# Performance work log

Hardware: AMD Instinct MI355X
Metric: run time of the kernel (lower is better)

## Reference

```python
import jax, jax.numpy as jnp
import numpy as np

B, H, S, D = 1, 16, 2048, 128
WINDOW = 512  # sliding-window size (SWA)
NEG = -1e9


def _swa_mask(s):
    # causal sliding-window additive mask: 0 where attended, -1e9 otherwise
    i = jnp.arange(s)[:, None]
    j = jnp.arange(s)[None, :]
    allowed = (j <= i) & (j > i - WINDOW)
    return jnp.where(allowed, 0.0, NEG).astype(jnp.float32)[None, None]  # [1,1,S,S]


def setup_inputs() -> dict:
    key = jax.random.key(0)
    kq, kk, kv = jax.random.split(key, 3)
    q = jax.random.normal(kq, (B, H, S, D), dtype=jnp.float32)
    k = jax.random.normal(kk, (B, H, S, D), dtype=jnp.float32)
    v = jax.random.normal(kv, (B, H, S, D), dtype=jnp.float32)
    mask = _swa_mask(S)
    return {"q": q, "k": k, "v": v, "mask": mask}


def reference(q, k, v, mask):
    # attn_w = q @ k^T + mask; softmax over kv; @ v  (no scaling, per source)
    attn_w = jnp.einsum("bhqd,bhkd->bhqk", q, k) + mask
    attn_w = jax.nn.softmax(attn_w, axis=-1)
    return jnp.einsum("bhqk,bhkd->bhqd", attn_w, v)
```

## Files before the change

kernel.cpp:

```cpp
#include <hip/hip_runtime.h>
#include <hip/hip_bf16.h>
#include <stdint.h>

#define H_NUM 16
#define S_LEN 2048
#define D_DIM 128
#define WIN   512
#define NWG   256
#define LOG2E 1.4426950408889634f

typedef __attribute__((ext_vector_type(8)))  _Float16 half8;
typedef __attribute__((ext_vector_type(2)))  __fp16   fp16x2;
typedef __attribute__((ext_vector_type(16))) float f32x16;
typedef __attribute__((ext_vector_type(4)))  unsigned int uint4v;

static __device__ __forceinline__ uint32_t pk16(float a, float b) {
    fp16x2 t = __builtin_amdgcn_cvt_pkrtz(a, b);
    return __builtin_bit_cast(uint32_t, t);
}
static __device__ __forceinline__ float fexp2(float x) {
#if __has_builtin(__builtin_amdgcn_exp2f)
    return __builtin_amdgcn_exp2f(x);
#else
    return exp2f(x);
#endif
}

__global__ __launch_bounds__(512, 2) void swa_fwd(
    const float* __restrict__ Q, const float* __restrict__ K,
    const float* __restrict__ V, float* __restrict__ O)
{
    __shared__ __align__(16) char arena[71680];
    char* ksL = arena;
    char* vsL = arena + 16384;
    char* ksH = arena + 32768;
    char* vsH = arena + 49152;
    float* mrg_o  = (float*)arena;
    float* mrg_ml = (float*)(arena + 69632);

    int bid = blockIdx.x;
    int wid = ((bid & 7) << 5) | (bid >> 3);
    int h    = wid >> 4;
    int q0wg = (wid & 15) << 7;

    int tid  = threadIdx.x;
    int wv   = tid >> 6;
    int lane = tid & 63;
    int qn = lane & 31;
    int hi = lane >> 5;
    int qsel = wv & 3;
    int hseg = wv >> 2;
    int q0 = q0wg + qsel * 32;

    const float* Qh = Q + ((size_t)h << 18);
    const float* Kg = K + ((size_t)h << 18);
    const float* Vg = V + ((size_t)h << 18);
    float*       Oh = O + ((size_t)h << 18);

    int tK_r = tid >> 4;
    int tK_d = (tid & 15) * 8;
    int tK_byte = tK_r * 256 + (((tid & 15) * 16) ^ ((tK_r & 7) << 4));
    int tV_d = (tid >> 4) * 4;
    int tV_s = (tid & 15) * 2;
    int tV_byte = (tV_s >> 3) * 2048 + tV_d * 16 + (tV_s & 7) * 2;

#define K_LOAD(A0, A1, KB_) do {                                               \
        const float* sp_ = Kg + ((size_t)((KB_) + tK_r) << 7) + tK_d;          \
        A0 = *reinterpret_cast<const float4*>(sp_);                            \
        A1 = *reinterpret_cast<const float4*>(sp_ + 4); } while (0)
#define K_WRITE(KS, BUF, A0, A1) do {                                          \
        uint4v u_;                                                             \
        u_[0] = pk16(A0.x, A0.y); u_[1] = pk16(A0.z, A0.w);                    \
        u_[2] = pk16(A1.x, A1.y); u_[3] = pk16(A1.z, A1.w);                    \
        *reinterpret_cast<uint4v*>((KS) + (BUF) * 8192 + tK_byte) = u_; } while (0)
#define V_LOAD(A0, A1, KB_) do {                                               \
        const float* sp_ = Vg + ((size_t)((KB_) + tV_s) << 7) + tV_d;          \
        A0 = *reinterpret_cast<const float4*>(sp_);                            \
        A1 = *reinterpret_cast<const float4*>(sp_ + D_DIM); } while (0)
#define V_WRITE(VS, BUF, A0, A1) do {                                          \
        char* b_ = (VS) + (BUF) * 8192 + tV_byte;                              \
        *reinterpret_cast<uint32_t*>(b_)      = pk16(A0.x, A1.x);              \
        *reinterpret_cast<uint32_t*>(b_ + 16) = pk16(A0.y, A1.y);              \
        *reinterpret_cast<uint32_t*>(b_ + 32) = pk16(A0.z, A1.z);              \
        *reinterpret_cast<uint32_t*>(b_ + 48) = pk16(A0.w, A1.w); } while (0)

    half8 qa[8];
    const float* qrow = Qh + ((size_t)(q0 + qn) << 7) + hi * 8;
    #pragma unroll
    for (int c = 0; c < 8; ++c) {
        float4 a0 = *reinterpret_cast<const float4*>(qrow + c * 16);
        float4 a1 = *reinterpret_cast<const float4*>(qrow + c * 16 + 4);
        qa[c] = (half8){(_Float16)(a0.x * LOG2E), (_Float16)(a0.y * LOG2E),
                        (_Float16)(a0.z * LOG2E), (_Float16)(a0.w * LOG2E),
                        (_Float16)(a1.x * LOG2E), (_Float16)(a1.y * LOG2E),
                        (_Float16)(a1.z * LOG2E), (_Float16)(a1.w * LOG2E)};
    }

    f32x16 oacc[4];
    #pragma unroll
    for (int db = 0; db < 4; ++db)
        #pragma unroll
        for (int i = 0; i < 16; ++i) oacc[db][i] = 0.f;
    float m_s = -1e30f, l_s = 0.f;

    int kstart = q0wg - (WIN - 1);
    if (kstart < 0) kstart = 0;
    kstart &= ~31;
    int nt  = ((q0wg + 128) - kstart) >> 5;
    int nt0 = (nt + 1) >> 1;
    int ntH = nt - nt0;
    int iq   = q0 + qn;
    int w_ks = q0 - (WIN - 1);
    int w_ke = q0 + 32;

    {
        float4 a0, a1;
        K_LOAD(a0, a1, kstart);             K_WRITE(ksL, 0, a0, a1);
        K_LOAD(a0, a1, kstart + nt0 * 32);  K_WRITE(ksH, 0, a0, a1);
        V_LOAD(a0, a1, kstart);             V_WRITE(vsL, 0, a0, a1);
        V_LOAD(a0, a1, kstart + nt0 * 32);  V_WRITE(vsH, 0, a0, a1);
    }

    int my_cnt = hseg ? ntH : nt0;
    for (int it = 0; it < nt0; ++it) {
        int cur = it & 1, nxt = cur ^ 1;
        __syncthreads();

        bool hl = (it + 1 < nt0), hh = (it + 1 < ntH);
        float4 kl0, kl1, kh0, kh1;
        if (hl) K_LOAD(kl0, kl1, kstart + (it + 1) * 32);
        if (hh) K_LOAD(kh0, kh1, kstart + (nt0 + it + 1) * 32);

        int mt = (hseg ? nt0 : 0) + it;
        int kb = kstart + mt * 32;
        bool act = (it < my_cnt) && (kb < w_ke) && (kb + 32 > w_ks);
        const char* ksb = (hseg ? ksH : ksL) + cur * 8192;
        const char* vsb = (hseg ? vsH : vsL) + cur * 8192;

        f32x16 sacc;
        if (act) {
            #pragma unroll
            for (int i = 0; i < 16; ++i) sacc[i] = 0.f;
            int sw = (qn & 7) << 4;
            #pragma unroll
            for (int c = 0; c < 8; ++c) {
                half8 kh = *reinterpret_cast<const half8*>(
                    ksb + qn * 256 + ((c * 32 + hi * 16) ^ sw));
                sacc = __builtin_amdgcn_mfma_f32_32x32x16_f16(kh, qa[c], sacc, 0, 0, 0);
            }
        }

        if (hl) K_WRITE(ksL, nxt, kl0, kl1);
        if (hh) K_WRITE(ksH, nxt, kh0, kh1);
        float4 vl0, vl1, vh0, vh1;
        if (hl) V_LOAD(vl0, vl1, kstart + (it + 1) * 32);
        if (hh) V_LOAD(vh0, vh1, kstart + (nt0 + it + 1) * 32);

        if (act) {
            float p[16];
            bool fullt = (kb >= q0 - 480) && (kb <= q0 - 31);
            if (fullt) {
                #pragma unroll
                for (int r = 0; r < 16; ++r) p[r] = sacc[r];
            } else {
                #pragma unroll
                for (int r = 0; r < 16; ++r) {
                    int j = kb + (r & 3) + 8 * (r >> 2) + 4 * hi;
                    p[r] = ((j <= iq) && (j + WIN > iq)) ? sacc[r] : -1e30f;
                }
            }
            float t0 = fmaxf(fmaxf(p[0], p[1]), p[2]);
            float t1 = fmaxf(fmaxf(p[3], p[4]), p[5]);
            float t2 = fmaxf(fmaxf(p[6], p[7]), p[8]);
            float t3 = fmaxf(fmaxf(p[9], p[10]), p[11]);
            float t4 = fmaxf(fmaxf(p[12], p[13]), p[14]);
            float tm = fmaxf(fmaxf(fmaxf(t0, t1), fmaxf(t2, t3)), fmaxf(t4, p[15]));
            tm = fmaxf(tm, __shfl_xor(tm, 32));

            if (!__all(tm - m_s <= 11.5424f)) {
                float mn = fmaxf(m_s, tm);
                float scale = fexp2(m_s - mn);
                m_s = mn;
                l_s *= scale;
                #pragma unroll
                for (int r = 0; r < 16; ++r) {
                    float sr = __shfl(scale, (r & 3) + 8 * (r >> 2) + 4 * hi);
                    oacc[0][r] *= sr; oacc[1][r] *= sr;
                    oacc[2][r] *= sr; oacc[3][r] *= sr;
                }
            }
            #pragma unroll
            for (int r = 0; r < 16; ++r) p[r] = fexp2(p[r] - m_s);
            {
                float s0 = (p[0] + p[1]) + (p[2] + p[3]);
                float s1 = (p[4] + p[5]) + (p[6] + p[7]);
                float s2 = (p[8] + p[9]) + (p[10] + p[11]);
                float s3 = (p[12] + p[13]) + (p[14] + p[15]);
                l_s += (s0 + s1) + (s2 + s3);
            }

            half8 pa[2];
            #pragma unroll
            for (int c = 0; c < 2; ++c) {
                uint32_t u0 = pk16(p[8*c+0], p[8*c+1]);
                uint32_t u1 = pk16(p[8*c+2], p[8*c+3]);
                uint32_t u2 = pk16(p[8*c+4], p[8*c+5]);
                uint32_t u3 = pk16(p[8*c+6], p[8*c+7]);
                uint4v fw;
#if __has_builtin(__builtin_amdgcn_permlane32_swap)
                auto w02 = __builtin_amdgcn_permlane32_swap(u0, u2, false, false);
                auto w13 = __builtin_amdgcn_permlane32_swap(u1, u3, false, false);
                fw[0] = (uint32_t)w02[0]; fw[2] = (uint32_t)w02[1];
                fw[1] = (uint32_t)w13[0]; fw[3] = (uint32_t)w13[1];
#else
                uint32_t x0 = (uint32_t)__shfl_xor((int)u0, 32);
                uint32_t x1 = (uint32_t)__shfl_xor((int)u1, 32);
                uint32_t x2 = (uint32_t)__shfl_xor((int)u2, 32);
                uint32_t x3 = (uint32_t)__shfl_xor((int)u3, 32);
                if (hi == 0) { fw[0] = u0; fw[1] = u1; fw[2] = x0; fw[3] = x1; }
                else         { fw[0] = x2; fw[1] = x3; fw[2] = u2; fw[3] = u3; }
#endif
                pa[c] = __builtin_bit_cast(half8, fw);
            }

            #pragma unroll
            for (int db = 0; db < 4; ++db)
                #pragma unroll
                for (int c = 0; c < 2; ++c) {
                    half8 vb8 = *reinterpret_cast<const half8*>(
                        vsb + (2 * c + hi) * 2048 + (db * 32 + qn) * 16);
                    oacc[db] = __builtin_amdgcn_mfma_f32_32x32x16_f16(pa[c], vb8, oacc[db], 0, 0, 0);
                }
        }

        if (hl) V_WRITE(vsL, nxt, vl0, vl1);
        if (hh) V_WRITE(vsH, nxt, vh0, vh1);
    }

    l_s += __shfl_xor(l_s, 32);
    __syncthreads();

    if (hseg == 1) {
        float* mo = mrg_o + (size_t)(qsel * 64 + lane) * 68;
        #pragma unroll
        for (int db = 0; db < 4; ++db)
            #pragma unroll
            for (int r = 0; r < 16; ++r) mo[db * 16 + r] = oacc[db][r];
        mrg_ml[(qsel * 64 + lane) * 2 + 0] = m_s;
        mrg_ml[(qsel * 64 + lane) * 2 + 1] = l_s;
    }
    __syncthreads();
    if (hseg == 0) {
        float m1 = mrg_ml[(qsel * 64 + lane) * 2 + 0];
        float l1 = mrg_ml[(qsel * 64 + lane) * 2 + 1];
        float mm = fmaxf(m_s, m1);
        float e0 = fexp2(m_s - mm);
        float e1 = fexp2(m1 - mm);
        float inv = 1.f / (l_s * e0 + l1 * e1);
        float sc0 = e0 * inv, sc1 = e1 * inv;
        const float* mo = mrg_o + (size_t)(qsel * 64 + lane) * 68;
        #pragma unroll
        for (int r = 0; r < 16; ++r) {
            int qr = (r & 3) + 8 * (r >> 2) + 4 * hi;
            float s0r = __shfl(sc0, qr);
            float s1r = __shfl(sc1, qr);
            float* orow = Oh + ((size_t)(q0 + qr) << 7) + qn;
            #pragma unroll
            for (int db = 0; db < 4; ++db)
                orow[db * 32] = oacc[db][r] * s0r + mo[db * 16 + r] * s1r;
        }
    }
#undef K_LOAD
#undef K_WRITE
#undef V_LOAD
#undef V_WRITE
}

extern "C" void kernel_launch(void* const* d_in, const int* in_sizes, int n_in,
                              void* d_out, int out_size, void* d_ws, size_t ws_size,
                              hipStream_t stream) {
    (void)in_sizes; (void)n_in; (void)out_size; (void)d_ws; (void)ws_size;
    const float* q = (const float*)d_in[0];
    const float* k = (const float*)d_in[1];
    const float* v = (const float*)d_in[2];
    float* o = (float*)d_out;
    hipLaunchKernelGGL(swa_fwd, dim3(NWG), dim3(512), 0, stream, q, k, v, o);
}
```

Before: 32.58 us.

## Process 64-key KV tiles per iteration instead of 32 in SWA kernel

Each loop iteration now loads, stages and consumes two 32-row K/V sub-tiles, for a 64-key tile. It issues two QK MFMA chains and four PV MFMA steps per d-block. This halves the number of barriers and loop iterations and gives more independent MFMA work between syncs. In exchange, LDS use grows to 128 KB, the kernel holds twice as many prefetch and probability registers under the same 512-thread launch bound (risking spills), and 64-alignment of the window start can add partially masked work.

Measured after the change: 54.87 us. +68.4%, slower.

```diff
diff --git a/kernel.cpp b/kernel.cpp
--- a/kernel.cpp
+++ b/kernel.cpp
@@ -30,11 +30,11 @@
     const float* __restrict__ Q, const float* __restrict__ K,
     const float* __restrict__ V, float* __restrict__ O)
 {
-    __shared__ __align__(16) char arena[71680];
+    __shared__ __align__(16) char arena[131072];
     char* ksL = arena;
-    char* vsL = arena + 16384;
-    char* ksH = arena + 32768;
-    char* vsH = arena + 49152;
+    char* vsL = arena + 32768;
+    char* ksH = arena + 65536;
+    char* vsH = arena + 98304;
     float* mrg_o  = (float*)arena;
     float* mrg_ml = (float*)(arena + 69632);
 
@@ -64,21 +64,21 @@
     int tV_s = (tid & 15) * 2;
     int tV_byte = (tV_s >> 3) * 2048 + tV_d * 16 + (tV_s & 7) * 2;
 
-#define K_LOAD(A0, A1, KB_) do {                                               \
-        const float* sp_ = Kg + ((size_t)((KB_) + tK_r) << 7) + tK_d;          \
+#define K_LOAD(A0, A1, KB_, SUB) do {                                          \
+        const float* sp_ = Kg + ((size_t)((KB_) + 32*(SUB) + tK_r) << 7) + tK_d;\
         A0 = *reinterpret_cast<const float4*>(sp_);                            \
         A1 = *reinterpret_cast<const float4*>(sp_ + 4); } while (0)
-#define K_WRITE(KS, BUF, A0, A1) do {                                          \
+#define K_WRITE(KS, BUF, A0, A1, SUB) do {                                     \
         uint4v u_;                                                             \
         u_[0] = pk16(A0.x, A0.y); u_[1] = pk16(A0.z, A0.w);                    \
         u_[2] = pk16(A1.x, A1.y); u_[3] = pk16(A1.z, A1.w);                    \
-        *reinterpret_cast<uint4v*>((KS) + (BUF) * 8192 + tK_byte) = u_; } while (0)
-#define V_LOAD(A0, A1, KB_) do {                                               \
-        const float* sp_ = Vg + ((size_t)((KB_) + tV_s) << 7) + tV_d;          \
+        *reinterpret_cast<uint4v*>((KS) + (BUF) * 16384 + (SUB) * 8192 + tK_byte) = u_; } while (0)
+#define V_LOAD(A0, A1, KB_, SUB) do {                                          \
+        const float* sp_ = Vg + ((size_t)((KB_) + 32*(SUB) + tV_s) << 7) + tV_d;\
         A0 = *reinterpret_cast<const float4*>(sp_);                            \
         A1 = *reinterpret_cast<const float4*>(sp_ + D_DIM); } while (0)
-#define V_WRITE(VS, BUF, A0, A1) do {                                          \
-        char* b_ = (VS) + (BUF) * 8192 + tV_byte;                              \
+#define V_WRITE(VS, BUF, A0, A1, SUB) do {                                     \
+        char* b_ = (VS) + (BUF) * 16384 + (SUB) * 8192 + tV_byte;              \
         *reinterpret_cast<uint32_t*>(b_)      = pk16(A0.x, A1.x);              \
         *reinterpret_cast<uint32_t*>(b_ + 16) = pk16(A0.y, A1.y);              \
         *reinterpret_cast<uint32_t*>(b_ + 32) = pk16(A0.z, A1.z);              \
@@ -105,8 +105,8 @@
 
     int kstart = q0wg - (WIN - 1);
     if (kstart < 0) kstart = 0;
-    kstart &= ~31;
-    int nt  = ((q0wg + 128) - kstart) >> 5;
+    kstart &= ~63;
+    int nt  = ((q0wg + 128) - kstart) >> 6;
     int nt0 = (nt + 1) >> 1;
     int ntH = nt - nt0;
     int iq   = q0 + qn;
@@ -115,10 +115,14 @@
 
     {
         float4 a0, a1;
-        K_LOAD(a0, a1, kstart);             K_WRITE(ksL, 0, a0, a1);
-        K_LOAD(a0, a1, kstart + nt0 * 32);  K_WRITE(ksH, 0, a0, a1);
-        V_LOAD(a0, a1, kstart);             V_WRITE(vsL, 0, a0, a1);
-        V_LOAD(a0, a1, kstart + nt0 * 32);  V_WRITE(vsH, 0, a0, a1);
+        K_LOAD(a0, a1, kstart, 0);             K_WRITE(ksL, 0, a0, a1, 0);
+        K_LOAD(a0, a1, kstart, 1);             K_WRITE(ksL, 0, a0, a1, 1);
+        K_LOAD(a0, a1, kstart + nt0 * 64, 0);  K_WRITE(ksH, 0, a0, a1, 0);
+        K_LOAD(a0, a1, kstart + nt0 * 64, 1);  K_WRITE(ksH, 0, a0, a1, 1);
+        V_LOAD(a0, a1, kstart, 0);             V_WRITE(vsL, 0, a0, a1, 0);
+        V_LOAD(a0, a1, kstart, 1);             V_WRITE(vsL, 0, a0, a1, 1);
+        V_LOAD(a0, a1, kstart + nt0 * 64, 0);  V_WRITE(vsH, 0, a0, a1, 0);
+        V_LOAD(a0, a1, kstart + nt0 * 64, 1);  V_WRITE(vsH, 0, a0, a1, 1);
     }
 
     int my_cnt = hseg ? ntH : nt0;
@@ -127,46 +131,64 @@
         __syncthreads();
 
         bool hl = (it + 1 < nt0), hh = (it + 1 < ntH);
-        float4 kl0, kl1, kh0, kh1;
-        if (hl) K_LOAD(kl0, kl1, kstart + (it + 1) * 32);
-        if (hh) K_LOAD(kh0, kh1, kstart + (nt0 + it + 1) * 32);
+        float4 kl0a, kl1a, kl0b, kl1b, kh0a, kh1a, kh0b, kh1b;
+        if (hl) { K_LOAD(kl0a, kl1a, kstart + (it + 1) * 64, 0);
+                  K_LOAD(kl0b, kl1b, kstart + (it + 1) * 64, 1); }
+        if (hh) { K_LOAD(kh0a, kh1a, kstart + (nt0 + it + 1) * 64, 0);
+                  K_LOAD(kh0b, kh1b, kstart + (nt0 + it + 1) * 64, 1); }
 
         int mt = (hseg ? nt0 : 0) + it;
-        int kb = kstart + mt * 32;
-        bool act = (it < my_cnt) && (kb < w_ke) && (kb + 32 > w_ks);
-        const char* ksb = (hseg ? ksH : ksL) + cur * 8192;
-        const char* vsb = (hseg ? vsH : vsL) + cur * 8192;
-
-        f32x16 sacc;
+        int kb = kstart + mt * 64;
+        bool act = (it < my_cnt) && (kb < w_ke) && (kb + 64 > w_ks);
+        const char* ksb = (hseg ? ksH : ksL) + cur * 16384;
+        const char* vsb = (hseg ? vsH : vsL) + cur * 16384;
+
+        f32x16 sacc0, sacc1;
         if (act) {
             #pragma unroll
-            for (int i = 0; i < 16; ++i) sacc[i] = 0.f;
+            for (int i = 0; i < 16; ++i) { sacc0[i] = 0.f; sacc1[i] = 0.f; }
             int sw = (qn & 7) << 4;
             #pragma unroll
             for (int c = 0; c < 8; ++c) {
-                half8 kh = *reinterpret_cast<const half8*>(
+                half8 ka = *reinterpret_cast<const half8*>(
                     ksb + qn * 256 + ((c * 32 + hi * 16) ^ sw));
-                sacc = __builtin_amdgcn_mfma_f32_32x32x16_f16(kh, qa[c], sacc, 0, 0, 0);
+                half8 kbq = *reinterpret_cast<const half8*>(
+                    ksb + 8192 + qn * 256 + ((c * 32 + hi * 16) ^ sw));
+                sacc0 = __builtin_amdgcn_mfma_f32_32x32x16_f16(ka,  qa[c], sacc0, 0, 0, 0);
+                sacc1 = __builtin_amdgcn_mfma_f32_32x32x16_f16(kbq, qa[c], sacc1, 0, 0, 0);
             }
         }
 
-        if (hl) K_WRITE(ksL, nxt, kl0, kl1);
-        if (hh) K_WRITE(ksH, nxt, kh0, kh1);
-        float4 vl0, vl1, vh0, vh1;
-        if (hl) V_LOAD(vl0, vl1, kstart + (it + 1) * 32);
-        if (hh) V_LOAD(vh0, vh1, kstart + (nt0 + it + 1) * 32);
+        if (hl) { K_WRITE(ksL, nxt, kl0a, kl1a, 0); K_WRITE(ksL, nxt, kl0b, kl1b, 1); }
+        if (hh) { K_WRITE(ksH, nxt, kh0a, kh1a, 0); K_WRITE(ksH, nxt, kh0b, kh1b, 1); }
+        float4 vl0a, vl1a, vl0b, vl1b, vh0a, vh1a, vh0b, vh1b;
+        if (hl) { V_LOAD(vl0a, vl1a, kstart + (it + 1) * 64, 0);
+                  V_LOAD(vl0b, vl1b, kstart + (it + 1) * 64, 1); }
+        if (hh) { V_LOAD(vh0a, vh1a, kstart + (nt0 + it + 1) * 64, 0);
+                  V_LOAD(vh0b, vh1b, kstart + (nt0 + it + 1) * 64, 1); }
 
         if (act) {
-            float p[16];
-            bool fullt = (kb >= q0 - 480) && (kb <= q0 - 31);
-            if (fullt) {
-                #pragma unroll
-                for (int r = 0; r < 16; ++r) p[r] = sacc[r];
+            float p[32];
+            bool full0 = (kb      >= q0 - 480) && (kb      <= q0 - 31);
+            bool full1 = (kb + 32 >= q0 - 480) && (kb + 32 <= q0 - 31);
+            if (full0) {
+                #pragma unroll
+                for (int r = 0; r < 16; ++r) p[r] = sacc0[r];
             } else {
                 #pragma unroll
                 for (int r = 0; r < 16; ++r) {
                     int j = kb + (r & 3) + 8 * (r >> 2) + 4 * hi;
-                    p[r] = ((j <= iq) && (j + WIN > iq)) ? sacc[r] : -1e30f;
+                    p[r] = ((j <= iq) && (j + WIN > iq)) ? sacc0[r] : -1e30f;
+                }
+            }
+            if (full1) {
+                #pragma unroll
+                for (int r = 0; r < 16; ++r) p[16 + r] = sacc1[r];
+            } else {
+                #pragma unroll
+                for (int r = 0; r < 16; ++r) {
+                    int j = kb + 32 + (r & 3) + 8 * (r >> 2) + 4 * hi;
+                    p[16 + r] = ((j <= iq) && (j + WIN > iq)) ? sacc1[r] : -1e30f;
                 }
             }
             float t0 = fmaxf(fmaxf(p[0], p[1]), p[2]);
@@ -174,7 +196,15 @@
             float t2 = fmaxf(fmaxf(p[6], p[7]), p[8]);
             float t3 = fmaxf(fmaxf(p[9], p[10]), p[11]);
             float t4 = fmaxf(fmaxf(p[12], p[13]), p[14]);
-            float tm = fmaxf(fmaxf(fmaxf(t0, t1), fmaxf(t2, t3)), fmaxf(t4, p[15]));
+            float t5 = fmaxf(fmaxf(p[15], p[16]), p[17]);
+            float t6 = fmaxf(fmaxf(p[18], p[19]), p[20]);
+            float t7 = fmaxf(fmaxf(p[21], p[22]), p[23]);
+            float t8 = fmaxf(fmaxf(p[24], p[25]), p[26]);
+            float t9 = fmaxf(fmaxf(p[27], p[28]), p[29]);
+            float ta = fmaxf(p[30], p[31]);
+            float tm = fmaxf(fmaxf(fmaxf(fmaxf(t0, t1), fmaxf(t2, t3)),
+                                   fmaxf(fmaxf(t4, t5), fmaxf(t6, t7))),
+                             fmaxf(fmaxf(t8, t9), ta));
             tm = fmaxf(tm, __shfl_xor(tm, 32));
 
             if (!__all(tm - m_s <= 11.5424f)) {
@@ -190,51 +220,60 @@
                 }
             }
             #pragma unroll
-            for (int r = 0; r < 16; ++r) p[r] = fexp2(p[r] - m_s);
+            for (int r = 0; r < 32; ++r) p[r] = fexp2(p[r] - m_s);
             {
                 float s0 = (p[0] + p[1]) + (p[2] + p[3]);
                 float s1 = (p[4] + p[5]) + (p[6] + p[7]);
                 float s2 = (p[8] + p[9]) + (p[10] + p[11]);
                 float s3 = (p[12] + p[13]) + (p[14] + p[15]);
-                l_s += (s0 + s1) + (s2 + s3);
-            }
-
-            half8 pa[2];
-            #pragma unroll
-            for (int c = 0; c < 2; ++c) {
-                uint32_t u0 = pk16(p[8*c+0], p[8*c+1]);
-                uint32_t u1 = pk16(p[8*c+2], p[8*c+3]);
-                uint32_t u2 = pk16(p[8*c+4], p[8*c+5]);
-                uint32_t u3 = pk16(p[8*c+6], p[8*c+7]);
-                uint4v fw;
+                float s4 = (p[16] + p[17]) + (p[18] + p[19]);
+                float s5 = (p[20] + p[21]) + (p[22] + p[23]);
+                float s6 = (p[24] + p[25]) + (p[26] + p[27]);
+                float s7 = (p[28] + p[29]) + (p[30] + p[31]);
+                l_s += ((s0 + s1) + (s2 + s3)) + ((s4 + s5) + (s6 + s7));
+            }
+
+            half8 pa[4];
+            #pragma unroll
+            for (int s = 0; s < 2; ++s)
+                #pragma unroll
+                for (int c = 0; c < 2; ++c) {
+                    const float* ps = p + 16 * s + 8 * c;
+                    uint32_t u0 = pk16(ps[0], ps[1]);
+                    uint32_t u1 = pk16(ps[2], ps[3]);
+                    uint32_t u2 = pk16(ps[4], ps[5]);
+                    uint32_t u3 = pk16(ps[6], ps[7]);
+                    uint4v fw;
 #if __has_builtin(__builtin_amdgcn_permlane32_swap)
-                auto w02 = __builtin_amdgcn_permlane32_swap(u0, u2, false, false);
-                auto w13 = __builtin_amdgcn_permlane32_swap(u1, u3, false, false);
-                fw[0] = (uint32_t)w02[0]; fw[2] = (uint32_t)w02[1];
-                fw[1] = (uint32_t)w13[0]; fw[3] = (uint32_t)w13[1];
+                    auto w02 = __builtin_amdgcn_permlane32_swap(u0, u2, false, false);
+                    auto w13 = __builtin_amdgcn_permlane32_swap(u1, u3, false, false);
+                    fw[0] = (uint32_t)w02[0]; fw[2] = (uint32_t)w02[1];
+                    fw[1] = (uint32_t)w13[0]; fw[3] = (uint32_t)w13[1];
 #else
-                uint32_t x0 = (uint32_t)__shfl_xor((int)u0, 32);
-                uint32_t x1 = (uint32_t)__shfl_xor((int)u1, 32);
-                uint32_t x2 = (uint32_t)__shfl_xor((int)u2, 32);
-                uint32_t x3 = (uint32_t)__shfl_xor((int)u3, 32);
-                if (hi == 0) { fw[0] = u0; fw[1] = u1; fw[2] = x0; fw[3] = x1; }
-                else         { fw[0] = x2; fw[1] = x3; fw[2] = u2; fw[3] = u3; }
+                    uint32_t x0 = (uint32_t)__shfl_xor((int)u0, 32);
+                    uint32_t x1 = (uint32_t)__shfl_xor((int)u1, 32);
+                    uint32_t x2 = (uint32_t)__shfl_xor((int)u2, 32);
+                    uint32_t x3 = (uint32_t)__shfl_xor((int)u3, 32);
+                    if (hi == 0) { fw[0] = u0; fw[1] = u1; fw[2] = x0; fw[3] = x1; }
+                    else         { fw[0] = x2; fw[1] = x3; fw[2] = u2; fw[3] = u3; }
 #endif
-                pa[c] = __builtin_bit_cast(half8, fw);
-            }
+                    pa[2 * s + c] = __builtin_bit_cast(half8, fw);
+                }
 
             #pragma unroll
             for (int db = 0; db < 4; ++db)
                 #pragma unroll
-                for (int c = 0; c < 2; ++c) {
-                    half8 vb8 = *reinterpret_cast<const half8*>(
-                        vsb + (2 * c + hi) * 2048 + (db * 32 + qn) * 16);
-                    oacc[db] = __builtin_amdgcn_mfma_f32_32x32x16_f16(pa[c], vb8, oacc[db], 0, 0, 0);
-                }
+                for (int s = 0; s < 2; ++s)
+                    #pragma unroll
+                    for (int c = 0; c < 2; ++c) {
+                        half8 vb8 = *reinterpret_cast<const half8*>(
+                            vsb + s * 8192 + (2 * c + hi) * 2048 + (db * 32 + qn) * 16);
+                        oacc[db] = __builtin_amdgcn_mfma_f32_32x32x16_f16(pa[2*s+c], vb8, oacc[db], 0, 0, 0);
+                    }
         }
 
-        if (hl) V_WRITE(vsL, nxt, vl0, vl1);
-        if (hh) V_WRITE(vsH, nxt, vh0, vh1);
+        if (hl) { V_WRITE(vsL, nxt, vl0a, vl1a, 0); V_WRITE(vsL, nxt, vl0b, vl1b, 1); }
+        if (hh) { V_WRITE(vsH, nxt, vh0a, vh1a, 0); V_WRITE(vsH, nxt, vh0b, vh1b, 1); }
     }
 
     l_s += __shfl_xor(l_s, 32);
```

## Software-pipeline QK^T of next tile with softmax/PV of previous tile

Applied to the files above, without the earlier changes.

Restructures the KV loop so that the QK^T MFMAs and the V register loads for tile i are issued alongside the softmax and PV MFMAs of tile i-1, with a final drain after the loop. The aim is to overlap matrix-core work with the exp/max vector work and to hide LDS latency by prefetching V into registers. In exchange it raises register pressure by keeping an extra score accumulator and 8 V fragments live, which may lower occupancy. It also removes the full-tile mask fast path and the lazy-rescale skip, so masking and rescaling now run on every tile.

Result: slower. 67.39 us (+106.8%).

```diff
diff --git a/kernel.cpp b/kernel.cpp
--- a/kernel.cpp
+++ b/kernel.cpp
@@ -113,6 +113,99 @@
     int w_ks = q0 - (WIN - 1);
     int w_ke = q0 + 32;
 
+    f32x16 saccP;
+    #pragma unroll
+    for (int i = 0; i < 16; ++i) saccP[i] = 0.f;
+    half8 vrP[8];
+    #pragma unroll
+    for (int i = 0; i < 8; ++i) vrP[i] = (half8)(_Float16)0.f;
+    bool actP = false;
+    int  kbP  = 0;
+
+    auto QKT = [&](const char* ksb) {
+        #pragma unroll
+        for (int i = 0; i < 16; ++i) saccP[i] = 0.f;
+        int sw = (qn & 7) << 4;
+        #pragma unroll
+        for (int c = 0; c < 8; ++c) {
+            half8 kh = *reinterpret_cast<const half8*>(
+                ksb + qn * 256 + ((c * 32 + hi * 16) ^ sw));
+            saccP = __builtin_amdgcn_mfma_f32_32x32x16_f16(kh, qa[c], saccP, 0, 0, 0);
+        }
+    };
+    auto VR = [&](const char* vsb) {
+        #pragma unroll
+        for (int db = 0; db < 4; ++db)
+            #pragma unroll
+            for (int c = 0; c < 2; ++c)
+                vrP[db * 2 + c] = *reinterpret_cast<const half8*>(
+                    vsb + (2 * c + hi) * 2048 + (db * 32 + qn) * 16);
+    };
+    auto FINISH = [&]() {
+        float p[16];
+        #pragma unroll
+        for (int r = 0; r < 16; ++r) {
+            int j = kbP + (r & 3) + 8 * (r >> 2) + 4 * hi;
+            p[r] = ((j <= iq) && (j + WIN > iq)) ? saccP[r] : -1e30f;
+        }
+        float t0 = fmaxf(fmaxf(p[0], p[1]), p[2]);
+        float t1 = fmaxf(fmaxf(p[3], p[4]), p[5]);
+        float t2 = fmaxf(fmaxf(p[6], p[7]), p[8]);
+        float t3 = fmaxf(fmaxf(p[9], p[10]), p[11]);
+        float t4 = fmaxf(fmaxf(p[12], p[13]), p[14]);
+        float tm = fmaxf(fmaxf(fmaxf(t0, t1), fmaxf(t2, t3)), fmaxf(t4, p[15]));
+        tm = fmaxf(tm, __shfl_xor(tm, 32));
+
+        float mn = fmaxf(m_s, tm);
+        float scale = fexp2(m_s - mn);
+        m_s = mn;
+        l_s *= scale;
+        #pragma unroll
+        for (int r = 0; r < 16; ++r) {
+            float sr = __shfl(scale, (r & 3) + 8 * (r >> 2) + 4 * hi);
+            oacc[0][r] *= sr; oacc[1][r] *= sr;
+            oacc[2][r] *= sr; oacc[3][r] *= sr;
+        }
+        #pragma unroll
+        for (int r = 0; r < 16; ++r) p[r] = fexp2(p[r] - m_s);
+        {
+            float s0 = (p[0] + p[1]) + (p[2] + p[3]);
+            float s1 = (p[4] + p[5]) + (p[6] + p[7]);
+            float s2 = (p[8] + p[9]) + (p[10] + p[11]);
+            float s3 = (p[12] + p[13]) + (p[14] + p[15]);
+            l_s += (s0 + s1) + (s2 + s3);
+        }
+        half8 pa[2];
+        #pragma unroll
+        for (int c = 0; c < 2; ++c) {
+            uint32_t u0 = pk16(p[8*c+0], p[8*c+1]);
+            uint32_t u1 = pk16(p[8*c+2], p[8*c+3]);
+            uint32_t u2 = pk16(p[8*c+4], p[8*c+5]);
+            uint32_t u3 = pk16(p[8*c+6], p[8*c+7]);
+            uint4v fw;
+#if __has_builtin(__builtin_amdgcn_permlane32_swap)
+            auto w02 = __builtin_amdgcn_permlane32_swap(u0, u2, false, false);
+            auto w13 = __builtin_amdgcn_permlane32_swap(u1, u3, false, false);
+            fw[0] = (uint32_t)w02[0]; fw[2] = (uint32_t)w02[1];
+            fw[1] = (uint32_t)w13[0]; fw[3] = (uint32_t)w13[1];
+#else
+            uint32_t x0 = (uint32_t)__shfl_xor((int)u0, 32);
+            uint32_t x1 = (uint32_t)__shfl_xor((int)u1, 32);
+            uint32_t x2 = (uint32_t)__shfl_xor((int)u2, 32);
+            uint32_t x3 = (uint32_t)__shfl_xor((int)u3, 32);
+            if (hi == 0) { fw[0] = u0; fw[1] = u1; fw[2] = x0; fw[3] = x1; }
+            else         { fw[0] = x2; fw[1] = x3; fw[2] = u2; fw[3] = u3; }
+#endif
+            pa[c] = __builtin_bit_cast(half8, fw);
+        }
+        #pragma unroll
+        for (int db = 0; db < 4; ++db)
+            #pragma unroll
+            for (int c = 0; c < 2; ++c)
+                oacc[db] = __builtin_amdgcn_mfma_f32_32x32x16_f16(
+                    pa[c], vrP[db * 2 + c], oacc[db], 0, 0, 0);
+    };
+
     {
         float4 a0, a1;
         K_LOAD(a0, a1, kstart);             K_WRITE(ksL, 0, a0, a1);
@@ -137,105 +230,27 @@
         const char* ksb = (hseg ? ksH : ksL) + cur * 8192;
         const char* vsb = (hseg ? vsH : vsL) + cur * 8192;
 
-        f32x16 sacc;
-        if (act) {
-            #pragma unroll
-            for (int i = 0; i < 16; ++i) sacc[i] = 0.f;
-            int sw = (qn & 7) << 4;
-            #pragma unroll
-            for (int c = 0; c < 8; ++c) {
-                half8 kh = *reinterpret_cast<const half8*>(
-                    ksb + qn * 256 + ((c * 32 + hi * 16) ^ sw));
-                sacc = __builtin_amdgcn_mfma_f32_32x32x16_f16(kh, qa[c], sacc, 0, 0, 0);
-            }
-        }
+        if (act && actP) {
+            FINISH();
+            QKT(ksb);
+            VR(vsb);
+            kbP = kb;
+        } else {
+            if (actP) FINISH();
+            if (act) { QKT(ksb); VR(vsb); kbP = kb; }
+        }
+        actP = act;
 
         if (hl) K_WRITE(ksL, nxt, kl0, kl1);
         if (hh) K_WRITE(ksH, nxt, kh0, kh1);
         float4 vl0, vl1, vh0, vh1;
         if (hl) V_LOAD(vl0, vl1, kstart + (it + 1) * 32);
         if (hh) V_LOAD(vh0, vh1, kstart + (nt0 + it + 1) * 32);
-
-        if (act) {
-            float p[16];
-            bool fullt = (kb >= q0 - 480) && (kb <= q0 - 31);
-            if (fullt) {
-                #pragma unroll
-                for (int r = 0; r < 16; ++r) p[r] = sacc[r];
-            } else {
-                #pragma unroll
-                for (int r = 0; r < 16; ++r) {
-                    int j = kb + (r & 3) + 8 * (r >> 2) + 4 * hi;
-                    p[r] = ((j <= iq) && (j + WIN > iq)) ? sacc[r] : -1e30f;
-                }
-            }
-            float t0 = fmaxf(fmaxf(p[0], p[1]), p[2]);
-            float t1 = fmaxf(fmaxf(p[3], p[4]), p[5]);
-            float t2 = fmaxf(fmaxf(p[6], p[7]), p[8]);
-            float t3 = fmaxf(fmaxf(p[9], p[10]), p[11]);
-            float t4 = fmaxf(fmaxf(p[12], p[13]), p[14]);
-            float tm = fmaxf(fmaxf(fmaxf(t0, t1), fmaxf(t2, t3)), fmaxf(t4, p[15]));
-            tm = fmaxf(tm, __shfl_xor(tm, 32));
-
-            if (!__all(tm - m_s <= 11.5424f)) {
-                float mn = fmaxf(m_s, tm);
-                float scale = fexp2(m_s - mn);
-                m_s = mn;
-                l_s *= scale;
-                #pragma unroll
-                for (int r = 0; r < 16; ++r) {
-                    float sr = __shfl(scale, (r & 3) + 8 * (r >> 2) + 4 * hi);
-                    oacc[0][r] *= sr; oacc[1][r] *= sr;
-                    oacc[2][r] *= sr; oacc[3][r] *= sr;
-                }
-            }
-            #pragma unroll
-            for (int r = 0; r < 16; ++r) p[r] = fexp2(p[r] - m_s);
-            {
-                float s0 = (p[0] + p[1]) + (p[2] + p[3]);
-                float s1 = (p[4] + p[5]) + (p[6] + p[7]);
-                float s2 = (p[8] + p[9]) + (p[10] + p[11]);
-                float s3 = (p[12] + p[13]) + (p[14] + p[15]);
-                l_s += (s0 + s1) + (s2 + s3);
-            }
-
-            half8 pa[2];
-            #pragma unroll
-            for (int c = 0; c < 2; ++c) {
-                uint32_t u0 = pk16(p[8*c+0], p[8*c+1]);
-                uint32_t u1 = pk16(p[8*c+2], p[8*c+3]);
-                uint32_t u2 = pk16(p[8*c+4], p[8*c+5]);
-                uint32_t u3 = pk16(p[8*c+6], p[8*c+7]);
-                uint4v fw;
-#if __has_builtin(__builtin_amdgcn_permlane32_swap)
-                auto w02 = __builtin_amdgcn_permlane32_swap(u0, u2, false, false);
-                auto w13 = __builtin_amdgcn_permlane32_swap(u1, u3, false, false);
-                fw[0] = (uint32_t)w02[0]; fw[2] = (uint32_t)w02[1];
-                fw[1] = (uint32_t)w13[0]; fw[3] = (uint32_t)w13[1];
-#else
-                uint32_t x0 = (uint32_t)__shfl_xor((int)u0, 32);
-                uint32_t x1 = (uint32_t)__shfl_xor((int)u1, 32);
-                uint32_t x2 = (uint32_t)__shfl_xor((int)u2, 32);
-                uint32_t x3 = (uint32_t)__shfl_xor((int)u3, 32);
-                if (hi == 0) { fw[0] = u0; fw[1] = u1; fw[2] = x0; fw[3] = x1; }
-                else         { fw[0] = x2; fw[1] = x3; fw[2] = u2; fw[3] = u3; }
-#endif
-                pa[c] = __builtin_bit_cast(half8, fw);
-            }
-
-            #pragma unroll
-            for (int db = 0; db < 4; ++db)
-                #pragma unroll
-                for (int c = 0; c < 2; ++c) {
-                    half8 vb8 = *reinterpret_cast<const half8*>(
-                        vsb + (2 * c + hi) * 2048 + (db * 32 + qn) * 16);
-                    oacc[db] = __builtin_amdgcn_mfma_f32_32x32x16_f16(pa[c], vb8, oacc[db], 0, 0, 0);
-                }
-        }
-
         if (hl) V_WRITE(vsL, nxt, vl0, vl1);
         if (hh) V_WRITE(vsH, nxt, vh0, vh1);
     }
+
+    if (actP) FINISH();
 
     l_s += __shfl_xor(l_s, 32);
     __syncthreads();
```
